# Optimization experiments

Measured on AMD Instinct MI355X. Metric: run time of the kernel, lower is better.

Reference implementation:

```python
import jax, jax.numpy as jnp
import numpy as np

EMBED_DIM = 2048
HEAD_DIM = 128


def setup_inputs() -> dict:
    key = jax.random.key(0)
    ks = jax.random.split(key, 7)
    B, S = 4, 2048
    lim = 1.0 / np.sqrt(EMBED_DIM)
    hidden_state = jax.random.normal(ks[0], (B, S, EMBED_DIM), dtype=jnp.float32)
    # nn.Linear weights stored as [out, in]; we keep [in, out] for x @ W
    Wq = jax.random.uniform(ks[1], (EMBED_DIM, HEAD_DIM), minval=-lim, maxval=lim, dtype=jnp.float32)
    Wk = jax.random.uniform(ks[2], (EMBED_DIM, HEAD_DIM), minval=-lim, maxval=lim, dtype=jnp.float32)
    Wv = jax.random.uniform(ks[3], (EMBED_DIM, HEAD_DIM), minval=-lim, maxval=lim, dtype=jnp.float32)
    bq = jax.random.uniform(ks[4], (HEAD_DIM,), minval=-lim, maxval=lim, dtype=jnp.float32)
    bk = jax.random.uniform(ks[5], (HEAD_DIM,), minval=-lim, maxval=lim, dtype=jnp.float32)
    bv = jax.random.uniform(ks[6], (HEAD_DIM,), minval=-lim, maxval=lim, dtype=jnp.float32)
    return {"hidden_state": hidden_state, "Wq": Wq, "bq": bq, "Wk": Wk, "bk": bk, "Wv": Wv, "bv": bv}


def reference(hidden_state, Wq, bq, Wk, bk, Wv, bv):
    q = hidden_state @ Wq + bq  # [B,S,D]
    k = hidden_state @ Wk + bk
    v = hidden_state @ Wv + bv
    scale = 1.0 / jnp.sqrt(jnp.asarray(HEAD_DIM, dtype=q.dtype))
    scores = jnp.einsum("bqd,bkd->bqk", q, k) * scale  # [B,S,S]
    S = q.shape[1]
    causal = jnp.triu(jnp.ones((S, S), dtype=bool), k=1)
    scores = jnp.where(causal, jnp.asarray(-1e10, dtype=scores.dtype), scores)
    weights = jax.nn.softmax(scores, axis=-1)
    return jnp.einsum("bqk,bkd->bqd", weights, v)
```

## Files before the change

### kernel.cpp

```cpp
#include <hip/hip_runtime.h>
#include <hip/hip_bf16.h>

#define EMBED 2048
#define SEQ   2048
#define BATCH 4
#define HD    128
#define MROWS (BATCH * SEQ)
#define NTOT  (3 * HD)
#define SCALE 0.08838834764831845f
#define NBQ   (SEQ / 64)
#define NSPL  6
#define FIXM  4.0f

typedef __attribute__((ext_vector_type(8))) short bf16x8;
typedef __attribute__((ext_vector_type(4))) float f32x4;

__device__ __forceinline__ unsigned short f2bf_rne(float x) {
    union { float f; unsigned u; } c; c.f = x;
    unsigned r = c.u + 0x7fffu + ((c.u >> 16) & 1u);
    return (unsigned short)(r >> 16);
}

__device__ __forceinline__ bf16x8 cvt8(f32x4 lo, f32x4 hi) {
    union { unsigned short s[8]; bf16x8 v; } u;
    u.s[0] = f2bf_rne(lo.x); u.s[1] = f2bf_rne(lo.y);
    u.s[2] = f2bf_rne(lo.z); u.s[3] = f2bf_rne(lo.w);
    u.s[4] = f2bf_rne(hi.x); u.s[5] = f2bf_rne(hi.y);
    u.s[6] = f2bf_rne(hi.z); u.s[7] = f2bf_rne(hi.w);
    return u.v;
}

#define MFMA16(a, b, c) __builtin_amdgcn_mfma_f32_16x16x32_bf16((a), (b), (c), 0, 0, 0)

__device__ __forceinline__ void gload_lds16(const void* gp, void* lp) {
    __builtin_amdgcn_global_load_lds(
        (const __attribute__((address_space(1))) void*)gp,
        (__attribute__((address_space(3))) void*)lp, 16, 0, 0);
}

__global__ __launch_bounds__(256) void wt_conv(
    const float* __restrict__ Wq, const float* __restrict__ Wk,
    const float* __restrict__ Wv, unsigned short* __restrict__ WT)
{
    __shared__ float lds[64][129];
    const int tid = threadIdx.x;
    const int blk = blockIdx.x;
    const int mat = blk >> 5;
    const int k0  = (blk & 31) * 64;
    const float* src = (mat == 0) ? Wq : (mat == 1) ? Wk : Wv;

    const float4* s4 = (const float4*)(src + (size_t)k0 * HD);
    for (int i = tid; i < 2048; i += 256) {
        const float4 v = s4[i];
        const int k  = i >> 5;
        const int n4 = (i & 31) * 4;
        lds[k][n4 + 0] = v.x; lds[k][n4 + 1] = v.y;
        lds[k][n4 + 2] = v.z; lds[k][n4 + 3] = v.w;
    }
    __syncthreads();

    const int n  = tid >> 1;
    const int kc = (tid & 1) * 32;
    unsigned short* dst = WT + ((size_t)(mat * HD + n)) * EMBED + k0 + kc;
#pragma unroll
    for (int c = 0; c < 4; ++c) {
        union { unsigned short s[8]; uint4 v; } u;
#pragma unroll
        for (int i = 0; i < 8; ++i)
            u.s[i] = f2bf_rne(lds[kc + c * 8 + i][n]);
        ((uint4*)dst)[c] = u.v;
    }
}

__global__ __launch_bounds__(256, 3) void gemm_qkv(
    const float* __restrict__ H, const unsigned short* __restrict__ WT,
    const float* __restrict__ bq, const float* __restrict__ bk,
    const float* __restrict__ bv,
    unsigned short* __restrict__ Qbf, unsigned short* __restrict__ Kbf,
    unsigned short* __restrict__ VT)
{
    __shared__ float          Abuf[4][64 * 32];
    __shared__ unsigned short Bbuf[4][64 * 32];

    const int tid  = threadIdx.x;
    const int w    = tid >> 6;
    const int lane = tid & 63;
    const int l16  = lane & 15;
    const int quad = lane >> 4;

    const int bid   = blockIdx.x;
    const int xcd   = bid & 7;
    const int local = bid >> 3;
    const int n_blk = local % 6;
    const int m_grp = local / 6;
    const int m0 = (m_grp * 8 + xcd) * 64;
    const int n0 = n_blk * 64;

    const float* agp[2]; int aoff[2];
#pragma unroll
    for (int i = 0; i < 2; ++i) {
        const int r = w * 16 + i * 8 + (lane >> 3);
        const int g = (lane & 7) ^ (lane >> 3);
        agp[i] = H + (size_t)(m0 + r) * EMBED + g * 4;
        aoff[i] = (w * 16 + i * 8) * 32;
    }
    const unsigned short* bgp =
        WT + (size_t)(n0 + w * 16 + (lane >> 2)) * EMBED
           + (((lane & 3) ^ ((lane >> 3) & 3)) * 8);
    const int boff = w * 512;

    const int wm = (w >> 1) * 32;
    const int wn = (w & 1) * 32;
    const int x7 = l16 & 7;
    const int x3 = (l16 >> 1) & 3;

    f32x4 acc[2][2];
#pragma unroll
    for (int mt = 0; mt < 2; ++mt)
#pragma unroll
        for (int nt = 0; nt < 2; ++nt) {
            f32x4 z = {0.f, 0.f, 0.f, 0.f};
            acc[mt][nt] = z;
        }

#define STAGE(bufi, kk) do {                                              \
        gload_lds16(agp[0] + (size_t)(kk) * 32, &Abuf[(bufi)][aoff[0]]);  \
        gload_lds16(agp[1] + (size_t)(kk) * 32, &Abuf[(bufi)][aoff[1]]);  \
        gload_lds16(bgp    + (size_t)(kk) * 32, &Bbuf[(bufi)][boff]);     \
    } while (0)

#define COMPUTE(bufi) do {                                                \
        bf16x8 aF[2], bF[2];                                              \
        _Pragma("unroll")                                                 \
        for (int mt = 0; mt < 2; ++mt) {                                  \
            const float* ab = &Abuf[(bufi)][(wm + mt * 16 + l16) * 32];   \
            const f32x4 lo = *(const f32x4*)(ab + (((2 * quad)     ^ x7) * 4)); \
            const f32x4 hi = *(const f32x4*)(ab + (((2 * quad + 1) ^ x7) * 4)); \
            aF[mt] = cvt8(lo, hi);                                        \
        }                                                                 \
        _Pragma("unroll")                                                 \
        for (int nt = 0; nt < 2; ++nt)                                    \
            bF[nt] = *(const bf16x8*)(                                    \
                &Bbuf[(bufi)][(wn + nt * 16 + l16) * 32 + ((quad ^ x3) * 8)]); \
        _Pragma("unroll")                                                 \
        for (int mt = 0; mt < 2; ++mt)                                    \
            _Pragma("unroll")                                             \
            for (int nt = 0; nt < 2; ++nt)                                \
                acc[mt][nt] = MFMA16(aF[mt], bF[nt], acc[mt][nt]);        \
    } while (0)

#define WAITBAR(n) do {                                                   \
        asm volatile("s_waitcnt vmcnt(" #n ")" ::: "memory");             \
        __builtin_amdgcn_s_barrier();                                     \
        __builtin_amdgcn_sched_barrier(0);                                \
    } while (0)

    STAGE(0, 0);
    STAGE(1, 1);
    STAGE(2, 2);

#pragma unroll 4
    for (int kt = 0; kt < 60; ++kt) {
        WAITBAR(6);
        STAGE((kt + 3) & 3, kt + 3);
        COMPUTE(kt & 3);
    }
    WAITBAR(6);
    STAGE(3, 63);
    COMPUTE(0);
    WAITBAR(6);
    COMPUTE(1);
    WAITBAR(3);
    COMPUTE(2);
    WAITBAR(0);
    COMPUTE(3);

#undef STAGE
#undef COMPUTE
#undef WAITBAR

#pragma unroll
    for (int nt = 0; nt < 2; ++nt) {
        const int col = n0 + wn + nt * 16 + l16;
        const int sel = col >> 7;
        const int c   = col & (HD - 1);
        const float bias = (sel == 0 ? bq : (sel == 1 ? bk : bv))[c];
#pragma unroll
        for (int mt = 0; mt < 2; ++mt) {
#pragma unroll
            for (int r = 0; r < 4; ++r) {
                const int row = m0 + wm + mt * 16 + quad * 4 + r;
                const float v = acc[mt][nt][r] + bias;
                if (sel == 0) {
                    Qbf[(size_t)row * HD + c] = f2bf_rne(v * SCALE);
                } else if (sel == 1) {
                    Kbf[(size_t)row * HD + c] = f2bf_rne(v);
                } else {
                    const int b = row >> 11;
                    const int s = row & (SEQ - 1);
                    VT[((size_t)b * HD + c) * SEQ + s] = f2bf_rne(v);
                }
            }
        }
    }
}

__global__ __launch_bounds__(256, 3) void flash_attn(
    const unsigned short* __restrict__ Qbf,
    const unsigned short* __restrict__ Kbf,
    const unsigned short* __restrict__ VT,
    float* __restrict__ pO, float* __restrict__ pL)
{
    __shared__ unsigned short Kbuf[64 * 128];
    __shared__ unsigned short Vbuf[128 * 64];
    __shared__ unsigned short plds[4][16 * 72];

    const int tid  = threadIdx.x;
    const int w    = tid >> 6;
    const int lane = tid & 63;
    const int l16  = lane & 15;
    const int quad = lane >> 4;
    const int b    = blockIdx.y;
    const int qb    = NBQ - 1 - blockIdx.x / NSPL;
    const int split = blockIdx.x % NSPL;
    const int q0    = qb * 64;
    const int qw0   = q0 + w * 16;

    bf16x8 aq[4];
    const unsigned short* qrow = Qbf + ((size_t)b * SEQ + qw0 + l16) * HD + quad * 8;
#pragma unroll
    for (int kt = 0; kt < 4; ++kt)
        aq[kt] = *(const bf16x8*)(qrow + kt * 32);

    f32x4 o[8];
#pragma unroll
    for (int nt = 0; nt < 8; ++nt) {
        f32x4 z = {0.f, 0.f, 0.f, 0.f};
        o[nt] = z;
    }
    float l_run[4];
#pragma unroll
    for (int r = 0; r < 4; ++r) l_run[r] = 0.f;

    const int lr4 = lane >> 4, sl4 = lane & 15;
    const int lr8 = lane >> 3, sl8 = lane & 7;
    const unsigned short* kbase = Kbf + (size_t)b * SEQ * HD;
    const unsigned short* vbase = VT + (size_t)b * HD * SEQ;
    unsigned short* myp = &plds[w][0];

    for (int t = split; t <= qb; t += NSPL) {
        const int j0 = t * 64;

#pragma unroll
        for (int i = 0; i < 4; ++i) {
            const int jl = w * 16 + i * 4 + lr4;
            gload_lds16(kbase + (size_t)(j0 + jl) * HD + (sl4 ^ (i * 4 + lr4)) * 8,
                        Kbuf + (w * 16 + i * 4) * 128);
        }
#pragma unroll
        for (int i = 0; i < 4; ++i) {
            const int dr = w * 32 + i * 8 + lr8;
            gload_lds16(vbase + (size_t)dr * SEQ + j0 + (sl8 ^ lr8) * 8,
                        Vbuf + (w * 32 + i * 8) * 64);
        }
        __syncthreads();

        if (j0 <= qw0 + 15) {
            f32x4 s[4];
#pragma unroll
            for (int nt = 0; nt < 4; ++nt) {
                f32x4 z = {0.f, 0.f, 0.f, 0.f};
                s[nt] = z;
            }
#pragma unroll
            for (int kt = 0; kt < 4; ++kt) {
#pragma unroll
                for (int nt = 0; nt < 4; ++nt) {
                    const bf16x8 bk = *(const bf16x8*)(
                        Kbuf + (nt * 16 + l16) * 128 + (((kt * 4 + quad) ^ l16) * 8));
                    s[nt] = MFMA16(aq[kt], bk, s[nt]);
                }
            }

#pragma unroll
            for (int nt = 0; nt < 4; ++nt) {
                const int j = j0 + nt * 16 + l16;
#pragma unroll
                for (int r = 0; r < 4; ++r) {
                    const int q = qw0 + quad * 4 + r;
                    const float sv = (j > q) ? -1e30f : s[nt][r];
                    const float pv = __expf(sv - FIXM);
                    l_run[r] += pv;
                    myp[(quad * 4 + r) * 72 + nt * 16 + l16] = f2bf_rne(pv);
                }
            }
            asm volatile("s_waitcnt lgkmcnt(0)" ::: "memory");
            const bf16x8 pf0 = *(const bf16x8*)(myp + l16 * 72 + quad * 8);
            const bf16x8 pf1 = *(const bf16x8*)(myp + l16 * 72 + 32 + quad * 8);

#pragma unroll
            for (int nt = 0; nt < 8; ++nt) {
                const bf16x8 bv0 = *(const bf16x8*)(
                    Vbuf + (nt * 16 + l16) * 64 + ((quad ^ (l16 & 7)) * 8));
                o[nt] = MFMA16(pf0, bv0, o[nt]);
            }
#pragma unroll
            for (int nt = 0; nt < 8; ++nt) {
                const bf16x8 bv1 = *(const bf16x8*)(
                    Vbuf + (nt * 16 + l16) * 64 + (((4 + quad) ^ (l16 & 7)) * 8));
                o[nt] = MFMA16(pf1, bv1, o[nt]);
            }
        }
        __syncthreads();
    }

#pragma unroll
    for (int r = 0; r < 4; ++r) {
#pragma unroll
        for (int d = 1; d < 16; d <<= 1)
            l_run[r] += __shfl_xor(l_run[r], d);
    }
    const int part = (b * NBQ + qb) * NSPL + split;
    float* po = pO + (size_t)part * (64 * HD);
#pragma unroll
    for (int nt = 0; nt < 8; ++nt)
#pragma unroll
        for (int r = 0; r < 4; ++r)
            po[(w * 16 + quad * 4 + r) * HD + nt * 16 + l16] = o[nt][r];
    if (l16 == 0) {
#pragma unroll
        for (int r = 0; r < 4; ++r)
            pL[part * 64 + w * 16 + quad * 4 + r] = l_run[r];
    }
}

__global__ __launch_bounds__(256) void attn_merge(
    const float* __restrict__ pO, const float* __restrict__ pL,
    float* __restrict__ out)
{
    const int bx  = blockIdx.x;
    const int b   = blockIdx.y;
    const int qb  = bx >> 3;
    const int tid = threadIdx.x;
    const int r   = (bx & 7) * 8 + (tid >> 5);
    const int d0  = (tid & 31) * 4;
    const int p0  = (b * NBQ + qb) * NSPL;

    float L = 0.f;
#pragma unroll
    for (int s = 0; s < NSPL; ++s) L += pL[(p0 + s) * 64 + r];
    const float invL = 1.0f / L;

    float4 acc = {0.f, 0.f, 0.f, 0.f};
#pragma unroll
    for (int s = 0; s < NSPL; ++s) {
        const float4 v = *(const float4*)(
            pO + (size_t)(p0 + s) * (64 * HD) + r * HD + d0);
        acc.x += v.x; acc.y += v.y; acc.z += v.z; acc.w += v.w;
    }
    float* op = out + ((size_t)b * SEQ + qb * 64 + r) * HD + d0;
    op[0] = acc.x * invL;
    op[1] = acc.y * invL;
    op[2] = acc.z * invL;
    op[3] = acc.w * invL;
}

extern "C" void kernel_launch(void* const* d_in, const int* in_sizes, int n_in,
                              void* d_out, int out_size, void* d_ws, size_t ws_size,
                              hipStream_t stream)
{
    const float* h  = (const float*)d_in[0];
    const float* Wq = (const float*)d_in[1];
    const float* bq = (const float*)d_in[2];
    const float* Wk = (const float*)d_in[3];
    const float* bk = (const float*)d_in[4];
    const float* Wv = (const float*)d_in[5];
    const float* bv = (const float*)d_in[6];
    float* out = (float*)d_out;

    float* pO = (float*)d_ws;
    float* pL = pO + (size_t)BATCH * NBQ * NSPL * 64 * HD;
    unsigned short* Qbf = (unsigned short*)(pL + (size_t)BATCH * NBQ * NSPL * 64);
    unsigned short* Kbf = Qbf + (size_t)MROWS * HD;
    unsigned short* VT  = Kbf + (size_t)MROWS * HD;
    unsigned short* WT  = VT  + (size_t)MROWS * HD;

    wt_conv<<<96, 256, 0, stream>>>(Wq, Wk, Wv, WT);
    gemm_qkv<<<768, 256, 0, stream>>>(h, WT, bq, bk, bv, Qbf, Kbf, VT);
    flash_attn<<<dim3(NBQ * NSPL, BATCH), 256, 0, stream>>>(Qbf, Kbf, VT, pO, pL);
    attn_merge<<<dim3(NBQ * 8, BATCH), 256, 0, stream>>>(pO, pL, out);
}
```

Baseline: 180.0 us.

## Restructure QKV GEMM to register-prefetch with bf16 LDS A tile and direct B loads

The QKV projection GEMM previously used a 4-stage global_load_lds pipeline with fp32 A and bf16 B tiles in LDS, and each wave converted A to bf16 on every read. It now prefetches A into registers, converts it to bf16 once and writes it into a padded, double-buffered LDS tile. B fragments are loaded straight from global memory into registers, double-buffered across iterations. This removes the duplicated fp32 to bf16 conversion work and the B staging in LDS, but it shortens the prefetch depth and duplicates B global loads across waves, which may expose more memory latency.

Result: slower. 186.6 us (+3.7%).

```diff
diff --git a/kernel.cpp b/kernel.cpp
--- a/kernel.cpp
+++ b/kernel.cpp
@@ -21,7 +21,7 @@
     return (unsigned short)(r >> 16);
 }
 
-__device__ __forceinline__ bf16x8 cvt8(f32x4 lo, f32x4 hi) {
+__device__ __forceinline__ bf16x8 cvt8(float4 lo, float4 hi) {
     union { unsigned short s[8]; bf16x8 v; } u;
     u.s[0] = f2bf_rne(lo.x); u.s[1] = f2bf_rne(lo.y);
     u.s[2] = f2bf_rne(lo.z); u.s[3] = f2bf_rne(lo.w);
@@ -79,8 +79,7 @@
     unsigned short* __restrict__ Qbf, unsigned short* __restrict__ Kbf,
     unsigned short* __restrict__ VT)
 {
-    __shared__ float          Abuf[4][64 * 32];
-    __shared__ unsigned short Bbuf[4][64 * 32];
+    __shared__ unsigned short Abuf[2][64 * 72];
 
     const int tid  = threadIdx.x;
     const int w    = tid >> 6;
@@ -96,23 +95,15 @@
     const int m0 = (m_grp * 8 + xcd) * 64;
     const int n0 = n_blk * 64;
 
-    const float* agp[2]; int aoff[2];
-#pragma unroll
-    for (int i = 0; i < 2; ++i) {
-        const int r = w * 16 + i * 8 + (lane >> 3);
-        const int g = (lane & 7) ^ (lane >> 3);
-        agp[i] = H + (size_t)(m0 + r) * EMBED + g * 4;
-        aoff[i] = (w * 16 + i * 8) * 32;
-    }
-    const unsigned short* bgp =
-        WT + (size_t)(n0 + w * 16 + (lane >> 2)) * EMBED
-           + (((lane & 3) ^ ((lane >> 3) & 3)) * 8);
-    const int boff = w * 512;
-
     const int wm = (w >> 1) * 32;
     const int wn = (w & 1) * 32;
-    const int x7 = l16 & 7;
-    const int x3 = (l16 >> 1) & 3;
+
+    const int arow = w * 16 + (lane >> 2);
+    const float* agp = H + (size_t)(m0 + arow) * EMBED + (lane & 3) * 16;
+    const int awoff = arow * 72 + (lane & 3) * 16;
+
+    const unsigned short* bga = WT + (size_t)(n0 + wn +      l16) * EMBED + quad * 8;
+    const unsigned short* bgb = WT + (size_t)(n0 + wn + 16 + l16) * EMBED + quad * 8;
 
     f32x4 acc[2][2];
 #pragma unroll
@@ -123,61 +114,67 @@
             acc[mt][nt] = z;
         }
 
-#define STAGE(bufi, kk) do {                                              \
-        gload_lds16(agp[0] + (size_t)(kk) * 32, &Abuf[(bufi)][aoff[0]]);  \
-        gload_lds16(agp[1] + (size_t)(kk) * 32, &Abuf[(bufi)][aoff[1]]);  \
-        gload_lds16(bgp    + (size_t)(kk) * 32, &Bbuf[(bufi)][boff]);     \
-    } while (0)
-
-#define COMPUTE(bufi) do {                                                \
-        bf16x8 aF[2], bF[2];                                              \
-        _Pragma("unroll")                                                 \
-        for (int mt = 0; mt < 2; ++mt) {                                  \
-            const float* ab = &Abuf[(bufi)][(wm + mt * 16 + l16) * 32];   \
-            const f32x4 lo = *(const f32x4*)(ab + (((2 * quad)     ^ x7) * 4)); \
-            const f32x4 hi = *(const f32x4*)(ab + (((2 * quad + 1) ^ x7) * 4)); \
-            aF[mt] = cvt8(lo, hi);                                        \
-        }                                                                 \
-        _Pragma("unroll")                                                 \
-        for (int nt = 0; nt < 2; ++nt)                                    \
-            bF[nt] = *(const bf16x8*)(                                    \
-                &Bbuf[(bufi)][(wn + nt * 16 + l16) * 32 + ((quad ^ x3) * 8)]); \
-        _Pragma("unroll")                                                 \
-        for (int mt = 0; mt < 2; ++mt)                                    \
-            _Pragma("unroll")                                             \
-            for (int nt = 0; nt < 2; ++nt)                                \
-                acc[mt][nt] = MFMA16(aF[mt], bF[nt], acc[mt][nt]);        \
-    } while (0)
-
-#define WAITBAR(n) do {                                                   \
-        asm volatile("s_waitcnt vmcnt(" #n ")" ::: "memory");             \
-        __builtin_amdgcn_s_barrier();                                     \
-        __builtin_amdgcn_sched_barrier(0);                                \
-    } while (0)
-
-    STAGE(0, 0);
-    STAGE(1, 1);
-    STAGE(2, 2);
-
-#pragma unroll 4
-    for (int kt = 0; kt < 60; ++kt) {
-        WAITBAR(6);
-        STAGE((kt + 3) & 3, kt + 3);
-        COMPUTE(kt & 3);
-    }
-    WAITBAR(6);
-    STAGE(3, 63);
-    COMPUTE(0);
-    WAITBAR(6);
-    COMPUTE(1);
-    WAITBAR(3);
-    COMPUTE(2);
-    WAITBAR(0);
-    COMPUTE(3);
-
-#undef STAGE
-#undef COMPUTE
-#undef WAITBAR
+    float4 a0, a1, a2, a3;
+    bf16x8 bP[2][2], bQ[2][2];
+
+#define STAGE_A(ktn) do {                                                  \
+        const float* ap_ = agp + (ktn) * 64;                               \
+        a0 = *(const float4*)(ap_);      a1 = *(const float4*)(ap_ + 4);   \
+        a2 = *(const float4*)(ap_ + 8);  a3 = *(const float4*)(ap_ + 12);  \
+    } while (0)
+
+#define STAGE_B(dst, ktn) do {                                             \
+        dst[0][0] = *(const bf16x8*)(bga + (ktn) * 64);                    \
+        dst[0][1] = *(const bf16x8*)(bga + (ktn) * 64 + 32);               \
+        dst[1][0] = *(const bf16x8*)(bgb + (ktn) * 64);                    \
+        dst[1][1] = *(const bf16x8*)(bgb + (ktn) * 64 + 32);               \
+    } while (0)
+
+#define WRITE_A(bufi) do {                                                 \
+        *(bf16x8*)(&Abuf[(bufi)][awoff])     = cvt8(a0, a1);               \
+        *(bf16x8*)(&Abuf[(bufi)][awoff + 8]) = cvt8(a2, a3);               \
+    } while (0)
+
+#define COMP(bufi, breg) do {                                              \
+        _Pragma("unroll")                                                  \
+        for (int ks = 0; ks < 2; ++ks) {                                   \
+            const bf16x8 aF0 = *(const bf16x8*)(                           \
+                &Abuf[(bufi)][(wm + l16) * 72 + (ks * 4 + quad) * 8]);     \
+            const bf16x8 aF1 = *(const bf16x8*)(                           \
+                &Abuf[(bufi)][(wm + 16 + l16) * 72 + (ks * 4 + quad) * 8]);\
+            acc[0][0] = MFMA16(aF0, breg[0][ks], acc[0][0]);               \
+            acc[0][1] = MFMA16(aF0, breg[1][ks], acc[0][1]);               \
+            acc[1][0] = MFMA16(aF1, breg[0][ks], acc[1][0]);               \
+            acc[1][1] = MFMA16(aF1, breg[1][ks], acc[1][1]);               \
+        }                                                                  \
+    } while (0)
+
+#define BODY(cur, kt, bCur, bNxt) do {                                     \
+        STAGE_A((kt) + 1);                                                 \
+        STAGE_B(bNxt, (kt) + 1);                                           \
+        COMP(cur, bCur);                                                   \
+        WRITE_A((cur) ^ 1);                                                \
+        __syncthreads();                                                   \
+    } while (0)
+
+    STAGE_A(0);
+    STAGE_B(bP, 0);
+    WRITE_A(0);
+    __syncthreads();
+
+#pragma unroll 1
+    for (int kp = 0; kp < 15; ++kp) {
+        BODY(0, 2 * kp,     bP, bQ);
+        BODY(1, 2 * kp + 1, bQ, bP);
+    }
+    BODY(0, 30, bP, bQ);
+    COMP(1, bQ);
+
+#undef STAGE_A
+#undef STAGE_B
+#undef WRITE_A
+#undef COMP
+#undef BODY
 
 #pragma unroll
     for (int nt = 0; nt < 2; ++nt) {
```

## Pre-convert hidden state to bf16 and widen QKV GEMM K-tile

Applied to the files above, without the earlier changes.

Adds blocks to the weight-conversion kernel that convert the fp32 hidden state to bf16 in the workspace. The QKV GEMM then streams bf16 A and B tiles with a K-step of 64 and drops the in-loop fp32-to-bf16 conversion, and its occupancy hint is lowered from 3 to 2 blocks. The aim is to cut per-tile ALU conversion work and halve the bytes the GEMM loads for A. In exchange it adds a full extra pass over the hidden state: a 64MB read and a 32MB write. The bf16 hidden-state buffer is aliased with the attention partial-output workspace, which is only safe because the buffer is dead before flash attention runs.

Result: faster. 170.3 us (-5.4%).

```diff
diff --git a/kernel.cpp b/kernel.cpp
--- a/kernel.cpp
+++ b/kernel.cpp
@@ -21,15 +21,6 @@
     return (unsigned short)(r >> 16);
 }
 
-__device__ __forceinline__ bf16x8 cvt8(f32x4 lo, f32x4 hi) {
-    union { unsigned short s[8]; bf16x8 v; } u;
-    u.s[0] = f2bf_rne(lo.x); u.s[1] = f2bf_rne(lo.y);
-    u.s[2] = f2bf_rne(lo.z); u.s[3] = f2bf_rne(lo.w);
-    u.s[4] = f2bf_rne(hi.x); u.s[5] = f2bf_rne(hi.y);
-    u.s[6] = f2bf_rne(hi.z); u.s[7] = f2bf_rne(hi.w);
-    return u.v;
-}
-
 #define MFMA16(a, b, c) __builtin_amdgcn_mfma_f32_16x16x32_bf16((a), (b), (c), 0, 0, 0)
 
 __device__ __forceinline__ void gload_lds16(const void* gp, void* lp) {
@@ -38,12 +29,28 @@
         (__attribute__((address_space(3))) void*)lp, 16, 0, 0);
 }
 
-__global__ __launch_bounds__(256) void wt_conv(
+__global__ __launch_bounds__(256) void conv_fused(
+    const float* __restrict__ H,
     const float* __restrict__ Wq, const float* __restrict__ Wk,
-    const float* __restrict__ Wv, unsigned short* __restrict__ WT)
+    const float* __restrict__ Wv,
+    unsigned short* __restrict__ Hbf, unsigned short* __restrict__ WT)
 {
     __shared__ float lds[64][129];
     const int tid = threadIdx.x;
+
+    if (blockIdx.x >= 96) {
+        const size_t i = ((size_t)(blockIdx.x - 96) * 256 + tid) * 8;
+        const float4 f0 = *(const float4*)(H + i);
+        const float4 f1 = *(const float4*)(H + i + 4);
+        union { unsigned short s[8]; uint4 v; } u;
+        u.s[0] = f2bf_rne(f0.x); u.s[1] = f2bf_rne(f0.y);
+        u.s[2] = f2bf_rne(f0.z); u.s[3] = f2bf_rne(f0.w);
+        u.s[4] = f2bf_rne(f1.x); u.s[5] = f2bf_rne(f1.y);
+        u.s[6] = f2bf_rne(f1.z); u.s[7] = f2bf_rne(f1.w);
+        *(uint4*)(Hbf + i) = u.v;
+        return;
+    }
+
     const int blk = blockIdx.x;
     const int mat = blk >> 5;
     const int k0  = (blk & 31) * 64;
@@ -72,15 +79,15 @@
     }
 }
 
-__global__ __launch_bounds__(256, 3) void gemm_qkv(
-    const float* __restrict__ H, const unsigned short* __restrict__ WT,
+__global__ __launch_bounds__(256, 2) void gemm_qkv(
+    const unsigned short* __restrict__ Hbf, const unsigned short* __restrict__ WT,
     const float* __restrict__ bq, const float* __restrict__ bk,
     const float* __restrict__ bv,
     unsigned short* __restrict__ Qbf, unsigned short* __restrict__ Kbf,
     unsigned short* __restrict__ VT)
 {
-    __shared__ float          Abuf[4][64 * 32];
-    __shared__ unsigned short Bbuf[4][64 * 32];
+    __shared__ unsigned short Abuf[4][64 * 64];
+    __shared__ unsigned short Bbuf[4][64 * 64];
 
     const int tid  = threadIdx.x;
     const int w    = tid >> 6;
@@ -96,23 +103,22 @@
     const int m0 = (m_grp * 8 + xcd) * 64;
     const int n0 = n_blk * 64;
 
-    const float* agp[2]; int aoff[2];
-#pragma unroll
-    for (int i = 0; i < 2; ++i) {
-        const int r = w * 16 + i * 8 + (lane >> 3);
-        const int g = (lane & 7) ^ (lane >> 3);
-        agp[i] = H + (size_t)(m0 + r) * EMBED + g * 4;
-        aoff[i] = (w * 16 + i * 8) * 32;
-    }
-    const unsigned short* bgp =
-        WT + (size_t)(n0 + w * 16 + (lane >> 2)) * EMBED
-           + (((lane & 3) ^ ((lane >> 3) & 3)) * 8);
-    const int boff = w * 512;
+    const int lr   = lane >> 3;
+    const int slot = lane & 7;
+    const int gch  = slot ^ lr;
+    const unsigned short* ag[2]; const unsigned short* bg[2];
+    int soff[2];
+#pragma unroll
+    for (int t = 0; t < 2; ++t) {
+        const int r = (w * 2 + t) * 8 + lr;
+        ag[t] = Hbf + (size_t)(m0 + r) * EMBED + gch * 8;
+        bg[t] = WT + (size_t)(n0 + r) * EMBED + gch * 8;
+        soff[t] = (w * 2 + t) * 512;
+    }
 
     const int wm = (w >> 1) * 32;
     const int wn = (w & 1) * 32;
-    const int x7 = l16 & 7;
-    const int x3 = (l16 >> 1) & 3;
+    const int xq = l16 & 7;
 
     f32x4 acc[2][2];
 #pragma unroll
@@ -123,54 +129,58 @@
             acc[mt][nt] = z;
         }
 
-#define STAGE(bufi, kk) do {                                              \
-        gload_lds16(agp[0] + (size_t)(kk) * 32, &Abuf[(bufi)][aoff[0]]);  \
-        gload_lds16(agp[1] + (size_t)(kk) * 32, &Abuf[(bufi)][aoff[1]]);  \
-        gload_lds16(bgp    + (size_t)(kk) * 32, &Bbuf[(bufi)][boff]);     \
+#define STAGE(bufi, kk) do {                                               \
+        _Pragma("unroll")                                                  \
+        for (int t = 0; t < 2; ++t) {                                      \
+            gload_lds16(ag[t] + (kk) * 64, &Abuf[(bufi)][soff[t]]);        \
+            gload_lds16(bg[t] + (kk) * 64, &Bbuf[(bufi)][soff[t]]);        \
+        }                                                                  \
     } while (0)
 
-#define COMPUTE(bufi) do {                                                \
-        bf16x8 aF[2], bF[2];                                              \
-        _Pragma("unroll")                                                 \
-        for (int mt = 0; mt < 2; ++mt) {                                  \
-            const float* ab = &Abuf[(bufi)][(wm + mt * 16 + l16) * 32];   \
-            const f32x4 lo = *(const f32x4*)(ab + (((2 * quad)     ^ x7) * 4)); \
-            const f32x4 hi = *(const f32x4*)(ab + (((2 * quad + 1) ^ x7) * 4)); \
-            aF[mt] = cvt8(lo, hi);                                        \
-        }                                                                 \
-        _Pragma("unroll")                                                 \
-        for (int nt = 0; nt < 2; ++nt)                                    \
-            bF[nt] = *(const bf16x8*)(                                    \
-                &Bbuf[(bufi)][(wn + nt * 16 + l16) * 32 + ((quad ^ x3) * 8)]); \
-        _Pragma("unroll")                                                 \
-        for (int mt = 0; mt < 2; ++mt)                                    \
-            _Pragma("unroll")                                             \
-            for (int nt = 0; nt < 2; ++nt)                                \
-                acc[mt][nt] = MFMA16(aF[mt], bF[nt], acc[mt][nt]);        \
+#define COMPUTE(bufi) do {                                                 \
+        bf16x8 aF[2][2], bF[2][2];                                         \
+        _Pragma("unroll")                                                  \
+        for (int mt = 0; mt < 2; ++mt)                                     \
+            _Pragma("unroll")                                              \
+            for (int ks = 0; ks < 2; ++ks)                                 \
+                aF[mt][ks] = *(const bf16x8*)(                             \
+                    &Abuf[(bufi)][0] + (wm + mt * 16 + l16) * 64           \
+                    + (((ks * 4 + quad) ^ xq) * 8));                       \
+        _Pragma("unroll")                                                  \
+        for (int nt = 0; nt < 2; ++nt)                                     \
+            _Pragma("unroll")                                              \
+            for (int ks = 0; ks < 2; ++ks)                                 \
+                bF[nt][ks] = *(const bf16x8*)(                             \
+                    &Bbuf[(bufi)][0] + (wn + nt * 16 + l16) * 64           \
+                    + (((ks * 4 + quad) ^ xq) * 8));                       \
+        _Pragma("unroll")                                                  \
+        for (int ks = 0; ks < 2; ++ks)                                     \
+            _Pragma("unroll")                                              \
+            for (int mt = 0; mt < 2; ++mt)                                 \
+                _Pragma("unroll")                                          \
+                for (int nt = 0; nt < 2; ++nt)                             \
+                    acc[mt][nt] = MFMA16(aF[mt][ks], bF[nt][ks], acc[mt][nt]); \
     } while (0)
 
-#define WAITBAR(n) do {                                                   \
-        asm volatile("s_waitcnt vmcnt(" #n ")" ::: "memory");             \
-        __builtin_amdgcn_s_barrier();                                     \
-        __builtin_amdgcn_sched_barrier(0);                                \
+#define WAITBAR(n) do {                                                    \
+        asm volatile("s_waitcnt vmcnt(" #n ")" ::: "memory");              \
+        __builtin_amdgcn_s_barrier();                                      \
+        __builtin_amdgcn_sched_barrier(0);                                 \
     } while (0)
 
     STAGE(0, 0);
     STAGE(1, 1);
     STAGE(2, 2);
 
-#pragma unroll 4
-    for (int kt = 0; kt < 60; ++kt) {
-        WAITBAR(6);
+#pragma unroll 1
+    for (int kt = 0; kt < 29; ++kt) {
+        WAITBAR(8);
         STAGE((kt + 3) & 3, kt + 3);
         COMPUTE(kt & 3);
     }
-    WAITBAR(6);
-    STAGE(3, 63);
-    COMPUTE(0);
-    WAITBAR(6);
+    WAITBAR(8);
     COMPUTE(1);
-    WAITBAR(3);
+    WAITBAR(4);
     COMPUTE(2);
     WAITBAR(0);
     COMPUTE(3);
@@ -378,15 +388,17 @@
     const float* bv = (const float*)d_in[6];
     float* out = (float*)d_out;
 
-    float* pO = (float*)d_ws;
-    float* pL = pO + (size_t)BATCH * NBQ * NSPL * 64 * HD;
-    unsigned short* Qbf = (unsigned short*)(pL + (size_t)BATCH * NBQ * NSPL * 64);
+    unsigned short* Hbf = (unsigned short*)d_ws;
+    unsigned short* Qbf = Hbf + (size_t)MROWS * EMBED;
     unsigned short* Kbf = Qbf + (size_t)MROWS * HD;
     unsigned short* VT  = Kbf + (size_t)MROWS * HD;
     unsigned short* WT  = VT  + (size_t)MROWS * HD;
-
-    wt_conv<<<96, 256, 0, stream>>>(Wq, Wk, Wv, WT);
-    gemm_qkv<<<768, 256, 0, stream>>>(h, WT, bq, bk, bv, Qbf, Kbf, VT);
+    float* pO  = (float*)d_ws;
+    float* pL  = pO + (size_t)BATCH * NBQ * NSPL * 64 * HD;
+
+    conv_fused<<<96 + (MROWS * EMBED) / (256 * 8), 256, 0, stream>>>(
+        h, Wq, Wk, Wv, Hbf, WT);
+    gemm_qkv<<<768, 256, 0, stream>>>(Hbf, WT, bq, bk, bv, Qbf, Kbf, VT);
     flash_attn<<<dim3(NBQ * NSPL, BATCH), 256, 0, stream>>>(Qbf, Kbf, VT, pO, pL);
     attn_merge<<<dim3(NBQ * 8, BATCH), 256, 0, stream>>>(pO, pL, out);
 }
```
